# Kernel tuning notes

Measured on AMD Instinct MI355X. Metric: run time of the kernel, lower is better.

## Reference

```python
import jax, jax.numpy as jnp
import numpy as np

WINDOW = 2  # window_size

def _causal_window_conv(x, W, b):
    # x: [B,T,D_in], W: [WINDOW, D_in, D_out], b: [D_out]
    # equivalent to left-padding x by WINDOW-1 zeros and a 'valid' conv
    B, T, _ = x.shape
    xp = jnp.pad(x, ((0, 0), (WINDOW - 1, 0), (0, 0)))  # [B, T+WINDOW-1, D_in]
    out = b
    for k in range(WINDOW):
        out = out + jnp.einsum('btd,de->bte', xp[:, k:k + T], W[k])
    return out  # [B,T,D_out]

def setup_inputs() -> dict:
    key = jax.random.key(0)
    ks = jax.random.split(key, 4)
    B, T, Din, Dout = 8, 4096, 256, 256
    scale = 0.05
    x = jax.random.normal(ks[0], (B, T, Din), dtype=jnp.float32)
    W_z = jax.random.normal(ks[1], (WINDOW, Din, Dout), dtype=jnp.float32) * scale
    W_f = jax.random.normal(ks[2], (WINDOW, Din, Dout), dtype=jnp.float32) * scale
    W_o = jax.random.normal(ks[3], (WINDOW, Din, Dout), dtype=jnp.float32) * scale
    b_z = jnp.zeros((Dout,), dtype=jnp.float32)
    b_f = jnp.zeros((Dout,), dtype=jnp.float32)
    b_o = jnp.zeros((Dout,), dtype=jnp.float32)
    return {"x": x, "W_z": W_z, "W_f": W_f, "W_o": W_o,
            "b_z": b_z, "b_f": b_f, "b_o": b_o}

def reference(x, W_z, W_f, W_o, b_z, b_f, b_o):
    # QRNN with fo-pooling (Bradbury et al. 2016), return_sequences=True
    z = jnp.tanh(_causal_window_conv(x, W_z, b_z))          # [B,T,D]
    f = jax.nn.sigmoid(_causal_window_conv(x, W_f, b_f))    # [B,T,D]
    o = jax.nn.sigmoid(_causal_window_conv(x, W_o, b_o))    # [B,T,D]

    def step(c, zfo):
        z_t, f_t, o_t = zfo
        c = f_t * c + (1.0 - f_t) * z_t   # fo-pooling recurrence
        h = o_t * c
        return c, h

    c0 = jnp.zeros(z.shape[::2], dtype=z.dtype)  # [B,D]
    # time-major for scan
    zfo = (z.transpose(1, 0, 2), f.transpose(1, 0, 2), o.transpose(1, 0, 2))
    _, hs = jax.lax.scan(step, c0, zfo)
    return hs.transpose(1, 0, 2)  # [B,T,D]
```

## Files before the change

kernel.cpp:

```cpp
#include <hip/hip_runtime.h>
#include <hip/hip_bf16.h>
#include <hip/hip_fp16.h>

#define BDIM 8
#define TDIM 4096
#define DDIM 256
#define MDIM (BDIM * TDIM)
#define NCHUNK 256
#define LCHUNK (TDIM / NCHUNK)

typedef _Float16 f16x8 __attribute__((ext_vector_type(8)));
typedef _Float16 f16x4 __attribute__((ext_vector_type(4)));
typedef float f32x4 __attribute__((ext_vector_type(4)));

__device__ __forceinline__ float sigmoid_(float x) {
    return 1.0f / (1.0f + __expf(-x));
}
__device__ __forceinline__ float tanh_(float x) {
    return 2.0f / (1.0f + __expf(-2.0f * x)) - 1.0f;
}

__device__ __forceinline__ f16x8 cvt8(const float4 a, const float4 b) {
    f16x8 r;
    r[0] = (_Float16)a.x; r[1] = (_Float16)a.y;
    r[2] = (_Float16)a.z; r[3] = (_Float16)a.w;
    r[4] = (_Float16)b.x; r[5] = (_Float16)b.y;
    r[6] = (_Float16)b.z; r[7] = (_Float16)b.w;
    return r;
}

__global__ __launch_bounds__(256) void convert_w(
    const float* __restrict__ Wz, const float* __restrict__ Wf,
    const float* __restrict__ Wo, _Float16* __restrict__ Wt) {
    const int idx = blockIdx.x * 256 + threadIdx.x;
    const int n = idx & 255;
    const int kin = (idx >> 8) & 255;
    const int w = (idx >> 16) & 1;
    const int g = idx >> 17;
    const float* W = (g == 0) ? Wz : (g == 1) ? Wf : Wo;
    const float v = W[(size_t)w * 65536 + (size_t)kin * 256 + n];
    Wt[((size_t)g * 256 + n) * 512 + w * 256 + kin] = (_Float16)v;
}

__global__ __launch_bounds__(256) void gates_mfma(
    const float* __restrict__ x, const _Float16* __restrict__ Wt,
    const float* __restrict__ bz, const float* __restrict__ bfv,
    const float* __restrict__ bo,
    _Float16* __restrict__ zbuf, _Float16* __restrict__ fbuf,
    _Float16* __restrict__ obuf) {
    const int gate = blockIdx.z;
    const int m0 = blockIdx.x * 128;
    const int n0 = blockIdx.y * 128;
    const int tid = threadIdx.x;
    const int lane = tid & 63;
    const int wave = tid >> 6;
    const int wr = wave >> 1;
    const int wc = wave & 1;

    __shared__ __align__(16) char smem[40960];

    const int arow = tid >> 1;
    const int ac = (tid & 1) * 16;

    const int b = m0 >> 12;
    const int t0 = m0 & (TDIM - 1);

    const float* xb = x + (size_t)b * TDIM * DDIM;
    const _Float16* pB = Wt + ((size_t)gate * 256 + n0 + arow) * 512 + ac;

    float4 ga0, ga1, ga2, ga3;
    int4 gb0, gb1;

#define LOAD_TILE(k0)                                                        \
    {                                                                        \
        const int half = (k0) >> 8;                                          \
        const int kin = (k0) & 255;                                          \
        const int t = t0 + arow - 1 + half;                                  \
        if (t >= 0) {                                                        \
            const float* src = xb + (size_t)t * DDIM + kin + ac;             \
            ga0 = *(const float4*)(src);                                     \
            ga1 = *(const float4*)(src + 4);                                 \
            ga2 = *(const float4*)(src + 8);                                 \
            ga3 = *(const float4*)(src + 12);                                \
        } else {                                                             \
            ga0 = ga1 = ga2 = ga3 = make_float4(0.f, 0.f, 0.f, 0.f);         \
        }                                                                    \
        gb0 = *(const int4*)(pB + (k0));                                     \
        gb1 = *(const int4*)(pB + (k0) + 8);                                 \
    }

#define STORE_TILE(bufp)                                                     \
    {                                                                        \
        _Float16* Ad = (_Float16*)(bufp);                                    \
        _Float16* Bd = (_Float16*)((char*)(bufp) + 8192);                    \
        *(f16x8*)(Ad + arow * 32 + ac) = cvt8(ga0, ga1);                     \
        *(f16x8*)(Ad + arow * 32 + ac + 8) = cvt8(ga2, ga3);                 \
        *(int4*)(Bd + arow * 32 + ac) = gb0;                                 \
        *(int4*)(Bd + arow * 32 + ac + 8) = gb1;                             \
    }

    f32x4 acc[4][4] = {};
    const int am = lane & 15;
    const int kq = (lane >> 4) * 8;

    LOAD_TILE(0);
    STORE_TILE(smem);

    for (int it = 0; it < 16; ++it) {
        __syncthreads();
        const int cur = it & 1;
        if (it < 15) LOAD_TILE((it + 1) * 32);

        const _Float16* Ab = (const _Float16*)(smem + cur * 16384);
        const _Float16* Bb = (const _Float16*)(smem + cur * 16384 + 8192);

        f16x8 a[4], bb[4];
#pragma unroll
        for (int i = 0; i < 4; ++i)
            a[i] = *(const f16x8*)(Ab + (wr * 64 + i * 16 + am) * 32 + kq);
#pragma unroll
        for (int j = 0; j < 4; ++j)
            bb[j] = *(const f16x8*)(Bb + (wc * 64 + j * 16 + am) * 32 + kq);
#pragma unroll
        for (int i = 0; i < 4; ++i)
#pragma unroll
            for (int j = 0; j < 4; ++j)
                acc[i][j] = __builtin_amdgcn_mfma_f32_16x16x32_f16(
                    a[i], bb[j], acc[i][j], 0, 0, 0);

        if (it < 15) STORE_TILE(smem + (cur ^ 1) * 16384);
    }

    __syncthreads();

    const float* bias = (gate == 0) ? bz : (gate == 1) ? bfv : bo;
    _Float16* outp = (gate == 0) ? zbuf : (gate == 1) ? fbuf : obuf;
    _Float16* eb = (_Float16*)smem + wave * 5120;
    const int rq = (lane >> 4) * 4;
#pragma unroll
    for (int j = 0; j < 4; ++j) {
        const int gc = n0 + wc * 64 + j * 16 + am;
        const float bj = bias[gc];
#pragma unroll
        for (int i = 0; i < 4; ++i) {
            f32x4 v = acc[i][j];
#pragma unroll
            for (int r = 0; r < 4; ++r) {
                const float val = v[r] + bj;
                const float act = (gate == 0) ? tanh_(val) : sigmoid_(val);
                eb[(i * 16 + rq + r) * 80 + j * 16 + am] = (_Float16)act;
            }
        }
    }
    __syncthreads();

    const int rrow = lane >> 3;
    const int rcol = (lane & 7) * 8;
#pragma unroll
    for (int rr = 0; rr < 8; ++rr) {
        const int row = rr * 8 + rrow;
        f16x8 v = *(const f16x8*)(eb + row * 80 + rcol);
        const size_t gm = (size_t)(m0 + wr * 64 + row);
        *(f16x8*)(outp + gm * DDIM + n0 + wc * 64 + rcol) = v;
    }
#undef LOAD_TILE
#undef STORE_TILE
}

__global__ __launch_bounds__(256) void scan_pass1(
    const _Float16* __restrict__ zbuf, const _Float16* __restrict__ fbuf,
    float* __restrict__ aggA, float* __restrict__ aggB) {
    const int idx = blockIdx.x * 256 + threadIdx.x;
    const int d8 = idx & 31;
    const int chunk = (idx >> 5) & (NCHUNK - 1);
    const int b = idx >> 13;

    const size_t row0 = (size_t)b * TDIM + (size_t)chunk * LCHUNK;
    const int4* zp = (const int4*)zbuf + row0 * 32 + d8;
    const int4* fp = (const int4*)fbuf + row0 * 32 + d8;

    float A[8], c[8];
#pragma unroll
    for (int e = 0; e < 8; ++e) { A[e] = 1.0f; c[e] = 0.0f; }

#pragma unroll
    for (int i = 0; i < LCHUNK; ++i) {
        int4 fv = *fp;
        int4 zv = *zp;
        const _Float16* fh = (const _Float16*)&fv;
        const _Float16* zh = (const _Float16*)&zv;
#pragma unroll
        for (int e = 0; e < 8; ++e) {
            const float f = (float)fh[e];
            const float z = (float)zh[e];
            A[e] *= f;
            c[e] = f * c[e] + (1.0f - f) * z;
        }
        fp += 32;
        zp += 32;
    }
    ((float4*)aggA)[(size_t)idx * 2 + 0] = make_float4(A[0], A[1], A[2], A[3]);
    ((float4*)aggA)[(size_t)idx * 2 + 1] = make_float4(A[4], A[5], A[6], A[7]);
    ((float4*)aggB)[(size_t)idx * 2 + 0] = make_float4(c[0], c[1], c[2], c[3]);
    ((float4*)aggB)[(size_t)idx * 2 + 1] = make_float4(c[4], c[5], c[6], c[7]);
}

__global__ __launch_bounds__(256) void carry_scan(
    const float* __restrict__ aggA, const float* __restrict__ aggB,
    float* __restrict__ carry) {
    const int g = blockIdx.x * 256 + threadIdx.x;
    const int d = g & 255;
    const int b = g >> 8;
    const size_t base = (size_t)b * NCHUNK * 256 + d;

    float c = 0.0f;
    for (int ch0 = 0; ch0 < NCHUNK; ch0 += 8) {
        float A[8], Bv[8];
#pragma unroll
        for (int u = 0; u < 8; ++u) {
            const size_t p = base + (size_t)(ch0 + u) * 256;
            A[u] = aggA[p];
            Bv[u] = aggB[p];
        }
#pragma unroll
        for (int u = 0; u < 8; ++u) {
            const size_t p = base + (size_t)(ch0 + u) * 256;
            carry[p] = c;
            c = A[u] * c + Bv[u];
        }
    }
}

__global__ __launch_bounds__(256) void scan_pass2(
    const _Float16* __restrict__ zbuf, const _Float16* __restrict__ fbuf,
    const _Float16* __restrict__ obuf, const float* __restrict__ carry,
    float* __restrict__ out) {
    const int idx = blockIdx.x * 256 + threadIdx.x;
    const int d8 = idx & 31;
    const int chunk = (idx >> 5) & (NCHUNK - 1);
    const int b = idx >> 13;

    float c[8];
    float4 c0 = ((const float4*)carry)[(size_t)idx * 2];
    float4 c1 = ((const float4*)carry)[(size_t)idx * 2 + 1];
    c[0] = c0.x; c[1] = c0.y; c[2] = c0.z; c[3] = c0.w;
    c[4] = c1.x; c[5] = c1.y; c[6] = c1.z; c[7] = c1.w;

    const size_t row0 = (size_t)b * TDIM + (size_t)chunk * LCHUNK;
    const int4* zp = (const int4*)zbuf + row0 * 32 + d8;
    const int4* fp = (const int4*)fbuf + row0 * 32 + d8;
    const int4* op = (const int4*)obuf + row0 * 32 + d8;
    float4* hp = (float4*)out + row0 * 64 + d8 * 2;

#pragma unroll
    for (int i = 0; i < LCHUNK; ++i) {
        int4 fv = *fp;
        int4 zv = *zp;
        int4 ov = *op;
        const _Float16* fh = (const _Float16*)&fv;
        const _Float16* zh = (const _Float16*)&zv;
        const _Float16* oh = (const _Float16*)&ov;
        float h[8];
#pragma unroll
        for (int e = 0; e < 8; ++e) {
            const float f = (float)fh[e];
            const float z = (float)zh[e];
            c[e] = f * c[e] + (1.0f - f) * z;
            h[e] = (float)oh[e] * c[e];
        }
        hp[0] = make_float4(h[0], h[1], h[2], h[3]);
        hp[1] = make_float4(h[4], h[5], h[6], h[7]);
        fp += 32;
        zp += 32;
        op += 32;
        hp += 64;
    }
}

extern "C" void kernel_launch(void* const* d_in, const int* in_sizes, int n_in,
                              void* d_out, int out_size, void* d_ws,
                              size_t ws_size, hipStream_t stream) {
    const float* x = (const float*)d_in[0];
    const float* Wz = (const float*)d_in[1];
    const float* Wf = (const float*)d_in[2];
    const float* Wo = (const float*)d_in[3];
    const float* bz = (const float*)d_in[4];
    const float* bfv = (const float*)d_in[5];
    const float* bo = (const float*)d_in[6];
    float* out = (float*)d_out;

    char* p = (char*)d_ws;
    _Float16* Wt = (_Float16*)p;    p += (size_t)3 * 256 * 512 * 2;
    _Float16* zbuf = (_Float16*)p;  p += (size_t)MDIM * DDIM * 2;
    _Float16* fbuf = (_Float16*)p;  p += (size_t)MDIM * DDIM * 2;
    _Float16* obuf = (_Float16*)p;  p += (size_t)MDIM * DDIM * 2;
    float* aggA = (float*)p;        p += (size_t)BDIM * NCHUNK * DDIM * 4;
    float* aggB = (float*)p;        p += (size_t)BDIM * NCHUNK * DDIM * 4;
    float* carry = (float*)p;

    convert_w<<<(3 * 2 * 256 * 256) / 256, 256, 0, stream>>>(Wz, Wf, Wo, Wt);

    gates_mfma<<<dim3(MDIM / 128, DDIM / 128, 3), 256, 0, stream>>>(
        x, Wt, bz, bfv, bo, zbuf, fbuf, obuf);

    scan_pass1<<<(BDIM * NCHUNK * 32) / 256, 256, 0, stream>>>(zbuf, fbuf,
                                                               aggA, aggB);
    carry_scan<<<(BDIM * DDIM) / 256, 256, 0, stream>>>(aggA, aggB, carry);
    scan_pass2<<<(BDIM * NCHUNK * 32) / 256, 256, 0, stream>>>(zbuf, fbuf,
                                                               obuf, carry, out);
}
```

Measured before the change: 181.3 us.

## Remap gate GEMM blocks for x-tile L2 reuse and shrink LDS footprint

Flattens the 3D grid into a 1D block index, so that the six (gate, n-half) blocks sharing an M tile are scheduled near each other and can reuse the same x rows from L2. Tile loads are reworked so each thread loads 8 contiguous elements from two rows 64 apart, which coalesces better. The epilogue is split into two passes with a smaller padded staging buffer, cutting shared memory from 40KB to 32KB to allow higher occupancy. The cost is an extra barrier pair in the epilogue and more index arithmetic.

New measurement: 186.3 us. 2.7% more time.

```diff
diff --git a/kernel.cpp b/kernel.cpp
--- a/kernel.cpp
+++ b/kernel.cpp
@@ -48,19 +48,23 @@
     const float* __restrict__ bo,
     _Float16* __restrict__ zbuf, _Float16* __restrict__ fbuf,
     _Float16* __restrict__ obuf) {
-    const int gate = blockIdx.z;
-    const int m0 = blockIdx.x * 128;
-    const int n0 = blockIdx.y * 128;
+    const int bid = blockIdx.x;
+    const int mt = (bid & 7) + 8 * (bid / 48);
+    const int g6 = (bid >> 3) % 6;
+    const int gate = g6 >> 1;
+    const int n0 = (g6 & 1) * 128;
+
+    const int m0 = mt * 128;
     const int tid = threadIdx.x;
     const int lane = tid & 63;
     const int wave = tid >> 6;
     const int wr = wave >> 1;
     const int wc = wave & 1;
 
-    __shared__ __align__(16) char smem[40960];
-
-    const int arow = tid >> 1;
-    const int ac = (tid & 1) * 16;
+    __shared__ __align__(16) char smem[32768];
+
+    const int arow = tid >> 2;
+    const int ac = (tid & 3) * 8;
 
     const int b = m0 >> 12;
     const int t0 = m0 & (TDIM - 1);
@@ -74,19 +78,21 @@
 #define LOAD_TILE(k0)                                                        \
     {                                                                        \
         const int half = (k0) >> 8;                                          \
-        const int kin = (k0) & 255;                                          \
-        const int t = t0 + arow - 1 + half;                                  \
-        if (t >= 0) {                                                        \
-            const float* src = xb + (size_t)t * DDIM + kin + ac;             \
-            ga0 = *(const float4*)(src);                                     \
-            ga1 = *(const float4*)(src + 4);                                 \
-            ga2 = *(const float4*)(src + 8);                                 \
-            ga3 = *(const float4*)(src + 12);                                \
+        const int kin = ((k0) & 255) + ac;                                   \
+        const int t1 = t0 + arow - 1 + half;                                 \
+        const int t2 = t1 + 64;                             \
+        if (t1 >= 0) {                                                       \
+            const float* s1 = xb + (size_t)t1 * DDIM + kin;                  \
+            ga0 = *(const float4*)(s1);                                      \
+            ga1 = *(const float4*)(s1 + 4);                                  \
         } else {                                                             \
-            ga0 = ga1 = ga2 = ga3 = make_float4(0.f, 0.f, 0.f, 0.f);         \
+            ga0 = ga1 = make_float4(0.f, 0.f, 0.f, 0.f);                     \
         }                                                                    \
+        const float* s2 = xb + (size_t)t2 * DDIM + kin;                      \
+        ga2 = *(const float4*)(s2);                                          \
+        ga3 = *(const float4*)(s2 + 4);                                      \
         gb0 = *(const int4*)(pB + (k0));                                     \
-        gb1 = *(const int4*)(pB + (k0) + 8);                                 \
+        gb1 = *(const int4*)(pB + (size_t)64 * 512 + (k0));                  \
     }
 
 #define STORE_TILE(bufp)                                                     \
@@ -94,9 +100,9 @@
         _Float16* Ad = (_Float16*)(bufp);                                    \
         _Float16* Bd = (_Float16*)((char*)(bufp) + 8192);                    \
         *(f16x8*)(Ad + arow * 32 + ac) = cvt8(ga0, ga1);                     \
-        *(f16x8*)(Ad + arow * 32 + ac + 8) = cvt8(ga2, ga3);                 \
+        *(f16x8*)(Ad + (arow + 64) * 32 + ac) = cvt8(ga2, ga3);              \
         *(int4*)(Bd + arow * 32 + ac) = gb0;                                 \
-        *(int4*)(Bd + arow * 32 + ac + 8) = gb1;                             \
+        *(int4*)(Bd + (arow + 64) * 32 + ac) = gb1;                          \
     }
 
     f32x4 acc[4][4] = {};
@@ -131,37 +137,40 @@
         if (it < 15) STORE_TILE(smem + (cur ^ 1) * 16384);
     }
 
-    __syncthreads();
-
     const float* bias = (gate == 0) ? bz : (gate == 1) ? bfv : bo;
     _Float16* outp = (gate == 0) ? zbuf : (gate == 1) ? fbuf : obuf;
-    _Float16* eb = (_Float16*)smem + wave * 5120;
+    _Float16* eb = (_Float16*)smem + wave * 2176;
     const int rq = (lane >> 4) * 4;
-#pragma unroll
-    for (int j = 0; j < 4; ++j) {
-        const int gc = n0 + wc * 64 + j * 16 + am;
-        const float bj = bias[gc];
-#pragma unroll
-        for (int i = 0; i < 4; ++i) {
-            f32x4 v = acc[i][j];
-#pragma unroll
-            for (int r = 0; r < 4; ++r) {
-                const float val = v[r] + bj;
-                const float act = (gate == 0) ? tanh_(val) : sigmoid_(val);
-                eb[(i * 16 + rq + r) * 80 + j * 16 + am] = (_Float16)act;
-            }
-        }
-    }
-    __syncthreads();
-
     const int rrow = lane >> 3;
     const int rcol = (lane & 7) * 8;
-#pragma unroll
-    for (int rr = 0; rr < 8; ++rr) {
-        const int row = rr * 8 + rrow;
-        f16x8 v = *(const f16x8*)(eb + row * 80 + rcol);
-        const size_t gm = (size_t)(m0 + wr * 64 + row);
-        *(f16x8*)(outp + gm * DDIM + n0 + wc * 64 + rcol) = v;
+
+#pragma unroll
+    for (int pass = 0; pass < 2; ++pass) {
+        __syncthreads();
+#pragma unroll
+        for (int j = 0; j < 4; ++j) {
+            const int gc = n0 + wc * 64 + j * 16 + am;
+            const float bj = bias[gc];
+#pragma unroll
+            for (int ii = 0; ii < 2; ++ii) {
+                f32x4 v = acc[pass * 2 + ii][j];
+#pragma unroll
+                for (int r = 0; r < 4; ++r) {
+                    const float val = v[r] + bj;
+                    const float act =
+                        (gate == 0) ? tanh_(val) : sigmoid_(val);
+                    eb[(ii * 16 + rq + r) * 68 + j * 16 + am] = (_Float16)act;
+                }
+            }
+        }
+        __syncthreads();
+#pragma unroll
+        for (int rr = 0; rr < 4; ++rr) {
+            const int row = rr * 8 + rrow;
+            f16x8 v = *(const f16x8*)(eb + row * 68 + rcol);
+            const size_t gm = (size_t)(m0 + wr * 64 + pass * 32 + row);
+            *(f16x8*)(outp + gm * DDIM + n0 + wc * 64 + rcol) = v;
+        }
     }
 #undef LOAD_TILE
 #undef STORE_TILE
@@ -300,7 +309,7 @@
 
     convert_w<<<(3 * 2 * 256 * 256) / 256, 256, 0, stream>>>(Wz, Wf, Wo, Wt);
 
-    gates_mfma<<<dim3(MDIM / 128, DDIM / 128, 3), 256, 0, stream>>>(
+    gates_mfma<<<(MDIM / 128) * 2 * 3, 256, 0, stream>>>(
         x, Wt, bz, bfv, bo, zbuf, fbuf, obuf);
 
     scan_pass1<<<(BDIM * NCHUNK * 32) / 256, 256, 0, stream>>>(zbuf, fbuf,
```

## Restructure gate GEMM as persistent kernel with LDS-resident weights and direct-register A loads

Applied to the files above, without the earlier changes.

Replaces the 128x128 double-buffered GEMM tile grid with a 256-block persistent kernel. Each block handles three 256x128 output tiles, stages a 128x256 half-precision weight slab in swizzled LDS per window tap, and streams x directly from global memory into registers for the MFMA A operand. The A loads are software-pipelined across k-steps, and tanh/sigmoid are unified into a single parameterised expression. This removes the A-tile LDS round trip and increases reuse per block. In exchange it uses larger accumulators (occupancy 1), uncoalesced row-strided A loads, and only 256 blocks.

After: 207.1 us. 1.14x slower.

```diff
diff --git a/kernel.cpp b/kernel.cpp
--- a/kernel.cpp
+++ b/kernel.cpp
@@ -10,14 +10,10 @@
 #define LCHUNK (TDIM / NCHUNK)
 
 typedef _Float16 f16x8 __attribute__((ext_vector_type(8)));
-typedef _Float16 f16x4 __attribute__((ext_vector_type(4)));
 typedef float f32x4 __attribute__((ext_vector_type(4)));
 
 __device__ __forceinline__ float sigmoid_(float x) {
     return 1.0f / (1.0f + __expf(-x));
-}
-__device__ __forceinline__ float tanh_(float x) {
-    return 2.0f / (1.0f + __expf(-2.0f * x)) - 1.0f;
 }
 
 __device__ __forceinline__ f16x8 cvt8(const float4 a, const float4 b) {
@@ -42,129 +38,155 @@
     Wt[((size_t)g * 256 + n) * 512 + w * 256 + kin] = (_Float16)v;
 }
 
-__global__ __launch_bounds__(256) void gates_mfma(
+__global__ __launch_bounds__(256, 1) void gates_mfma(
     const float* __restrict__ x, const _Float16* __restrict__ Wt,
     const float* __restrict__ bz, const float* __restrict__ bfv,
     const float* __restrict__ bo,
     _Float16* __restrict__ zbuf, _Float16* __restrict__ fbuf,
     _Float16* __restrict__ obuf) {
-    const int gate = blockIdx.z;
-    const int m0 = blockIdx.x * 128;
-    const int n0 = blockIdx.y * 128;
     const int tid = threadIdx.x;
     const int lane = tid & 63;
     const int wave = tid >> 6;
-    const int wr = wave >> 1;
-    const int wc = wave & 1;
-
-    __shared__ __align__(16) char smem[40960];
-
-    const int arow = tid >> 1;
-    const int ac = (tid & 1) * 16;
-
-    const int b = m0 >> 12;
-    const int t0 = m0 & (TDIM - 1);
-
-    const float* xb = x + (size_t)b * TDIM * DDIM;
-    const _Float16* pB = Wt + ((size_t)gate * 256 + n0 + arow) * 512 + ac;
-
-    float4 ga0, ga1, ga2, ga3;
-    int4 gb0, gb1;
-
-#define LOAD_TILE(k0)                                                        \
+
+    __shared__ __align__(16) char smem[65536];
+    _Float16* Bs = (_Float16*)smem;
+
+    const int am = lane & 15;
+    const int lq = lane >> 4;
+    const int kq = lq * 8;
+    const int amx = am & 7;
+
+    const int scol = tid & 127;
+    const int sck = (tid >> 7) * 16;
+
+    for (int jr = 0; jr < 3; ++jr) {
+        const int j = blockIdx.x + jr * 256;
+        const int gate = j >> 8;
+        const int n0 = ((j >> 7) & 1) * 128;
+        const int m0 = (j & 127) * 256;
+        const int b = m0 >> 12;
+        const int t0 = m0 & (TDIM - 1);
+        const float* xb = x + (size_t)b * TDIM * DDIM;
+
+        f32x4 acc[4][8] = {};
+
+        const int twave = t0 + wave * 64;
+        const bool edge = (t0 == 0) && (wave == 0);
+
+        for (int pass = 0; pass < 2; ++pass) {
+            __syncthreads();
+            {
+                const _Float16* src =
+                    Wt + ((size_t)gate * 256 + n0 + scol) * 512 + pass * 256 +
+                    sck * 8;
+                int4 r[16];
+#pragma unroll
+                for (int i = 0; i < 16; ++i) r[i] = ((const int4*)src)[i];
+                _Float16* dstc = Bs + scol * 256;
+#pragma unroll
+                for (int i = 0; i < 16; ++i)
+                    *(int4*)(dstc + (((sck + i) ^ (scol & 7)) << 3)) = r[i];
+            }
+            __syncthreads();
+
+            const float* arow[4];
+#pragma unroll
+            for (int rf = 0; rf < 4; ++rf)
+                arow[rf] = xb +
+                           ((long)(twave + rf * 16 + am) - 1 + pass) * DDIM +
+                           kq;
+            const bool ep = edge && (pass == 0);
+
+            float4 A0[4][2], A1[4][2];
+
+#define LOADA(dst, ks8)                                                      \
     {                                                                        \
-        const int half = (k0) >> 8;                                          \
-        const int kin = (k0) & 255;                                          \
-        const int t = t0 + arow - 1 + half;                                  \
-        if (t >= 0) {                                                        \
-            const float* src = xb + (size_t)t * DDIM + kin + ac;             \
-            ga0 = *(const float4*)(src);                                     \
-            ga1 = *(const float4*)(src + 4);                                 \
-            ga2 = *(const float4*)(src + 8);                                 \
-            ga3 = *(const float4*)(src + 12);                                \
-        } else {                                                             \
-            ga0 = ga1 = ga2 = ga3 = make_float4(0.f, 0.f, 0.f, 0.f);         \
+        const int kb = (ks8)*32;                                             \
+        _Pragma("unroll") for (int rf = 0; rf < 4; ++rf) {                   \
+            dst[rf][0] = *(const float4*)(arow[rf] + kb);                    \
+            dst[rf][1] = *(const float4*)(arow[rf] + kb + 4);                 \
         }                                                                    \
-        gb0 = *(const int4*)(pB + (k0));                                     \
-        gb1 = *(const int4*)(pB + (k0) + 8);                                 \
-    }
-
-#define STORE_TILE(bufp)                                                     \
+    }
+#define LOADA_EDGE(dst, ks8)                                                 \
     {                                                                        \
-        _Float16* Ad = (_Float16*)(bufp);                                    \
-        _Float16* Bd = (_Float16*)((char*)(bufp) + 8192);                    \
-        *(f16x8*)(Ad + arow * 32 + ac) = cvt8(ga0, ga1);                     \
-        *(f16x8*)(Ad + arow * 32 + ac + 8) = cvt8(ga2, ga3);                 \
-        *(int4*)(Bd + arow * 32 + ac) = gb0;                                 \
-        *(int4*)(Bd + arow * 32 + ac + 8) = gb1;                             \
-    }
-
-    f32x4 acc[4][4] = {};
-    const int am = lane & 15;
-    const int kq = (lane >> 4) * 8;
-
-    LOAD_TILE(0);
-    STORE_TILE(smem);
-
-    for (int it = 0; it < 16; ++it) {
+        const int kb = (ks8)*32;                                             \
+        _Pragma("unroll") for (int rf = 0; rf < 4; ++rf) {                   \
+            if (rf == 0 && am == 0) {                                        \
+                dst[rf][0] = make_float4(0.f, 0.f, 0.f, 0.f);                \
+                dst[rf][1] = make_float4(0.f, 0.f, 0.f, 0.f);                \
+            } else {                                                         \
+                dst[rf][0] = *(const float4*)(arow[rf] + kb);                \
+                dst[rf][1] = *(const float4*)(arow[rf] + kb + 4);             \
+            }                                                                \
+        }                                                                    \
+    }
+#define DOMFMA(Abuf, ks8)                                                    \
+    {                                                                        \
+        f16x8 bb[8];                                                         \
+        _Pragma("unroll") for (int cf = 0; cf < 8; ++cf) {                   \
+            const int col = cf * 16 + am;                                    \
+            const int ch = ((ks8)*4 + lq) ^ amx;                             \
+            bb[cf] = *(const f16x8*)(Bs + col * 256 + ch * 8);               \
+        }                                                                    \
+        f16x8 aa[4];                                                         \
+        _Pragma("unroll") for (int rf = 0; rf < 4; ++rf) aa[rf] =            \
+            cvt8(Abuf[rf][0], Abuf[rf][1]);                                  \
+        _Pragma("unroll") for (int rf = 0; rf < 4; ++rf)                     \
+            _Pragma("unroll") for (int cf = 0; cf < 8; ++cf) acc[rf][cf] =   \
+                __builtin_amdgcn_mfma_f32_16x16x32_f16(aa[rf], bb[cf],       \
+                                                       acc[rf][cf], 0, 0, 0);\
+    }
+
+            if (ep) { LOADA_EDGE(A0, 0) } else { LOADA(A0, 0) }
+            for (int ks8 = 0; ks8 < 8; ks8 += 2) {
+                if (ep) { LOADA_EDGE(A1, ks8 + 1) } else { LOADA(A1, ks8 + 1) }
+                DOMFMA(A0, ks8)
+                if (ks8 + 2 < 8) {
+                    if (ep) { LOADA_EDGE(A0, ks8 + 2) } else { LOADA(A0, ks8 + 2) }
+                }
+                DOMFMA(A1, ks8 + 1)
+            }
+#undef LOADA
+#undef LOADA_EDGE
+#undef DOMFMA
+        }
+
         __syncthreads();
-        const int cur = it & 1;
-        if (it < 15) LOAD_TILE((it + 1) * 32);
-
-        const _Float16* Ab = (const _Float16*)(smem + cur * 16384);
-        const _Float16* Bb = (const _Float16*)(smem + cur * 16384 + 8192);
-
-        f16x8 a[4], bb[4];
-#pragma unroll
-        for (int i = 0; i < 4; ++i)
-            a[i] = *(const f16x8*)(Ab + (wr * 64 + i * 16 + am) * 32 + kq);
-#pragma unroll
-        for (int j = 0; j < 4; ++j)
-            bb[j] = *(const f16x8*)(Bb + (wc * 64 + j * 16 + am) * 32 + kq);
-#pragma unroll
-        for (int i = 0; i < 4; ++i)
-#pragma unroll
-            for (int j = 0; j < 4; ++j)
-                acc[i][j] = __builtin_amdgcn_mfma_f32_16x16x32_f16(
-                    a[i], bb[j], acc[i][j], 0, 0, 0);
-
-        if (it < 15) STORE_TILE(smem + (cur ^ 1) * 16384);
-    }
-
-    __syncthreads();
-
-    const float* bias = (gate == 0) ? bz : (gate == 1) ? bfv : bo;
-    _Float16* outp = (gate == 0) ? zbuf : (gate == 1) ? fbuf : obuf;
-    _Float16* eb = (_Float16*)smem + wave * 5120;
-    const int rq = (lane >> 4) * 4;
-#pragma unroll
-    for (int j = 0; j < 4; ++j) {
-        const int gc = n0 + wc * 64 + j * 16 + am;
-        const float bj = bias[gc];
-#pragma unroll
-        for (int i = 0; i < 4; ++i) {
-            f32x4 v = acc[i][j];
-#pragma unroll
-            for (int r = 0; r < 4; ++r) {
-                const float val = v[r] + bj;
-                const float act = (gate == 0) ? tanh_(val) : sigmoid_(val);
-                eb[(i * 16 + rq + r) * 80 + j * 16 + am] = (_Float16)act;
+        const float* bias = (gate == 0) ? bz : (gate == 1) ? bfv : bo;
+        _Float16* outp = (gate == 0) ? zbuf : (gate == 1) ? fbuf : obuf;
+        const float amul = (gate == 0) ? 2.f : 1.f;
+        const float smul = (gate == 0) ? -2.f : -1.f;
+        const float asub = (gate == 0) ? 1.f : 0.f;
+
+        _Float16* eb = (_Float16*)smem + wave * 8192;
+        float bj[8];
+#pragma unroll
+        for (int cf = 0; cf < 8; ++cf) bj[cf] = bias[n0 + cf * 16 + am];
+        const int rq = lq * 4;
+#pragma unroll
+        for (int rf = 0; rf < 4; ++rf)
+#pragma unroll
+            for (int cf = 0; cf < 8; ++cf) {
+                f32x4 v = acc[rf][cf];
+#pragma unroll
+                for (int r = 0; r < 4; ++r) {
+                    const float val = v[r] + bj[cf];
+                    const float act =
+                        amul / (1.f + __expf(smul * val)) - asub;
+                    eb[(rf * 16 + rq + r) * 128 + cf * 16 + am] =
+                        (_Float16)act;
+                }
             }
-        }
-    }
-    __syncthreads();
-
-    const int rrow = lane >> 3;
-    const int rcol = (lane & 7) * 8;
-#pragma unroll
-    for (int rr = 0; rr < 8; ++rr) {
-        const int row = rr * 8 + rrow;
-        f16x8 v = *(const f16x8*)(eb + row * 80 + rcol);
-        const size_t gm = (size_t)(m0 + wr * 64 + row);
-        *(f16x8*)(outp + gm * DDIM + n0 + wc * 64 + rcol) = v;
-    }
-#undef LOAD_TILE
-#undef STORE_TILE
+#pragma unroll
+        for (int i = 0; i < 16; ++i) {
+            const int flat = i * 64 + lane;
+            const int row = flat >> 4;
+            const int ch = flat & 15;
+            f16x8 v = *(const f16x8*)(eb + row * 128 + ch * 8);
+            *(f16x8*)(outp + (size_t)(m0 + wave * 64 + row) * DDIM + n0 +
+                      ch * 8) = v;
+        }
+    }
 }
 
 __global__ __launch_bounds__(256) void scan_pass1(
@@ -300,8 +322,7 @@
 
     convert_w<<<(3 * 2 * 256 * 256) / 256, 256, 0, stream>>>(Wz, Wf, Wo, Wt);
 
-    gates_mfma<<<dim3(MDIM / 128, DDIM / 128, 3), 256, 0, stream>>>(
-        x, Wt, bz, bfv, bo, zbuf, fbuf, obuf);
+    gates_mfma<<<256, 256, 0, stream>>>(x, Wt, bz, bfv, bo, zbuf, fbuf, obuf);
 
     scan_pass1<<<(BDIM * NCHUNK * 32) / 256, 256, 0, stream>>>(zbuf, fbuf,
                                                                aggA, aggB);
```

## Fuse three-pass chunked scan into single decoupled-lookback scan kernel

Applied to the files above, without the earlier changes.

Replaces the three scan kernels (chunk aggregate, serial carry scan, and apply) with one kernel. Each block handles 128 timesteps of one batch across all 256 features, publishes its aggregate and an inclusive prefix through flags, and looks back over earlier chunks to get its entering state. This removes two kernel launches and the aggA/carry round trips, but adds a hipMemsetAsync for the flags. It relies on forward-progress ordering of blocks (only 256 blocks) and drops parallelism from 2048 to 256 blocks with scalar fp16 loads, which may lower bandwidth use.

Result: slower. 401.0 us (+121.2%).

```diff
diff --git a/kernel.cpp b/kernel.cpp
--- a/kernel.cpp
+++ b/kernel.cpp
@@ -6,11 +6,10 @@
 #define TDIM 4096
 #define DDIM 256
 #define MDIM (BDIM * TDIM)
-#define NCHUNK 256
-#define LCHUNK (TDIM / NCHUNK)
+#define SCHUNK 128
+#define NCH (TDIM / SCHUNK)
 
 typedef _Float16 f16x8 __attribute__((ext_vector_type(8)));
-typedef _Float16 f16x4 __attribute__((ext_vector_type(4)));
 typedef float f32x4 __attribute__((ext_vector_type(4)));
 
 __device__ __forceinline__ float sigmoid_(float x) {
@@ -167,113 +166,100 @@
 #undef STORE_TILE
 }
 
-__global__ __launch_bounds__(256) void scan_pass1(
+__global__ __launch_bounds__(256) void scan_fused(
     const _Float16* __restrict__ zbuf, const _Float16* __restrict__ fbuf,
-    float* __restrict__ aggA, float* __restrict__ aggB) {
-    const int idx = blockIdx.x * 256 + threadIdx.x;
-    const int d8 = idx & 31;
-    const int chunk = (idx >> 5) & (NCHUNK - 1);
-    const int b = idx >> 13;
-
-    const size_t row0 = (size_t)b * TDIM + (size_t)chunk * LCHUNK;
-    const int4* zp = (const int4*)zbuf + row0 * 32 + d8;
-    const int4* fp = (const int4*)fbuf + row0 * 32 + d8;
-
-    float A[8], c[8];
-#pragma unroll
-    for (int e = 0; e < 8; ++e) { A[e] = 1.0f; c[e] = 0.0f; }
-
-#pragma unroll
-    for (int i = 0; i < LCHUNK; ++i) {
-        int4 fv = *fp;
-        int4 zv = *zp;
-        const _Float16* fh = (const _Float16*)&fv;
-        const _Float16* zh = (const _Float16*)&zv;
-#pragma unroll
-        for (int e = 0; e < 8; ++e) {
-            const float f = (float)fh[e];
-            const float z = (float)zh[e];
-            A[e] *= f;
-            c[e] = f * c[e] + (1.0f - f) * z;
-        }
-        fp += 32;
-        zp += 32;
-    }
-    ((float4*)aggA)[(size_t)idx * 2 + 0] = make_float4(A[0], A[1], A[2], A[3]);
-    ((float4*)aggA)[(size_t)idx * 2 + 1] = make_float4(A[4], A[5], A[6], A[7]);
-    ((float4*)aggB)[(size_t)idx * 2 + 0] = make_float4(c[0], c[1], c[2], c[3]);
-    ((float4*)aggB)[(size_t)idx * 2 + 1] = make_float4(c[4], c[5], c[6], c[7]);
-}
-
-__global__ __launch_bounds__(256) void carry_scan(
-    const float* __restrict__ aggA, const float* __restrict__ aggB,
-    float* __restrict__ carry) {
-    const int g = blockIdx.x * 256 + threadIdx.x;
-    const int d = g & 255;
-    const int b = g >> 8;
-    const size_t base = (size_t)b * NCHUNK * 256 + d;
-
-    float c = 0.0f;
-    for (int ch0 = 0; ch0 < NCHUNK; ch0 += 8) {
-        float A[8], Bv[8];
-#pragma unroll
-        for (int u = 0; u < 8; ++u) {
-            const size_t p = base + (size_t)(ch0 + u) * 256;
-            A[u] = aggA[p];
-            Bv[u] = aggB[p];
-        }
-#pragma unroll
-        for (int u = 0; u < 8; ++u) {
-            const size_t p = base + (size_t)(ch0 + u) * 256;
-            carry[p] = c;
-            c = A[u] * c + Bv[u];
-        }
-    }
-}
-
-__global__ __launch_bounds__(256) void scan_pass2(
-    const _Float16* __restrict__ zbuf, const _Float16* __restrict__ fbuf,
-    const _Float16* __restrict__ obuf, const float* __restrict__ carry,
-    float* __restrict__ out) {
-    const int idx = blockIdx.x * 256 + threadIdx.x;
-    const int d8 = idx & 31;
-    const int chunk = (idx >> 5) & (NCHUNK - 1);
-    const int b = idx >> 13;
-
-    float c[8];
-    float4 c0 = ((const float4*)carry)[(size_t)idx * 2];
-    float4 c1 = ((const float4*)carry)[(size_t)idx * 2 + 1];
-    c[0] = c0.x; c[1] = c0.y; c[2] = c0.z; c[3] = c0.w;
-    c[4] = c1.x; c[5] = c1.y; c[6] = c1.z; c[7] = c1.w;
-
-    const size_t row0 = (size_t)b * TDIM + (size_t)chunk * LCHUNK;
-    const int4* zp = (const int4*)zbuf + row0 * 32 + d8;
-    const int4* fp = (const int4*)fbuf + row0 * 32 + d8;
-    const int4* op = (const int4*)obuf + row0 * 32 + d8;
-    float4* hp = (float4*)out + row0 * 64 + d8 * 2;
-
-#pragma unroll
-    for (int i = 0; i < LCHUNK; ++i) {
-        int4 fv = *fp;
-        int4 zv = *zp;
-        int4 ov = *op;
-        const _Float16* fh = (const _Float16*)&fv;
-        const _Float16* zh = (const _Float16*)&zv;
-        const _Float16* oh = (const _Float16*)&ov;
-        float h[8];
-#pragma unroll
-        for (int e = 0; e < 8; ++e) {
-            const float f = (float)fh[e];
-            const float z = (float)zh[e];
-            c[e] = f * c[e] + (1.0f - f) * z;
-            h[e] = (float)oh[e] * c[e];
-        }
-        hp[0] = make_float4(h[0], h[1], h[2], h[3]);
-        hp[1] = make_float4(h[4], h[5], h[6], h[7]);
-        fp += 32;
-        zp += 32;
-        op += 32;
-        hp += 64;
+    const _Float16* __restrict__ obuf, float* __restrict__ aggA,
+    float* __restrict__ aggB, float* __restrict__ aggI,
+    int* __restrict__ flags, float* __restrict__ out) {
+    const int bid = blockIdx.x;
+    const int b = bid >> 5;
+    const int chunk = bid & (NCH - 1);
+    const int d = threadIdx.x;
+    const size_t base = ((size_t)b * TDIM + (size_t)chunk * SCHUNK) * DDIM + d;
+
+    float A = 1.0f, c = 0.0f;
+    for (int i = 0; i < SCHUNK; i += 4) {
+        float ff[4], zz[4];
+#pragma unroll
+        for (int u = 0; u < 4; ++u) {
+            ff[u] = (float)fbuf[base + (size_t)(i + u) * DDIM];
+            zz[u] = (float)zbuf[base + (size_t)(i + u) * DDIM];
+        }
+#pragma unroll
+        for (int u = 0; u < 4; ++u) {
+            A *= ff[u];
+            c = ff[u] * c + (1.0f - ff[u]) * zz[u];
+        }
+    }
+
+    __shared__ int st_sh;
+    float c_enter = 0.0f;
+
+    if (chunk == 0) {
+        aggI[bid * 256 + d] = c;
+        __threadfence();
+        __syncthreads();
+        if (d == 0)
+            __hip_atomic_store(&flags[bid], 2, __ATOMIC_RELEASE,
+                               __HIP_MEMORY_SCOPE_AGENT);
+    } else {
+        aggA[bid * 256 + d] = A;
+        aggB[bid * 256 + d] = c;
+        __threadfence();
+        __syncthreads();
+        if (d == 0)
+            __hip_atomic_store(&flags[bid], 1, __ATOMIC_RELEASE,
+                               __HIP_MEMORY_SCOPE_AGENT);
+
+        float accA = 1.0f, accB = 0.0f;
+        for (int j = chunk - 1; j >= 0; --j) {
+            if (d == 0) {
+                int s;
+                do {
+                    s = __hip_atomic_load(&flags[(b << 5) + j],
+                                          __ATOMIC_ACQUIRE,
+                                          __HIP_MEMORY_SCOPE_AGENT);
+                    if (s == 0) __builtin_amdgcn_s_sleep(1);
+                } while (s == 0);
+                st_sh = s;
+            }
+            __syncthreads();
+            const int s = st_sh;
+            __threadfence();
+            if (s == 2) {
+                const float v = aggI[((b << 5) + j) * 256 + d];
+                c_enter = accA * v + accB;
+                break;
+            }
+            const float Aj = aggA[((b << 5) + j) * 256 + d];
+            const float Bj = aggB[((b << 5) + j) * 256 + d];
+            accB = accB + accA * Bj;
+            accA = accA * Aj;
+            __syncthreads();
+        }
+
+        aggI[bid * 256 + d] = A * c_enter + c;
+        __threadfence();
+        __syncthreads();
+        if (d == 0)
+            __hip_atomic_store(&flags[bid], 2, __ATOMIC_RELEASE,
+                               __HIP_MEMORY_SCOPE_AGENT);
+    }
+
+    float c2 = c_enter;
+    for (int i = 0; i < SCHUNK; i += 4) {
+        float ff[4], zz[4], oo[4];
+#pragma unroll
+        for (int u = 0; u < 4; ++u) {
+            ff[u] = (float)fbuf[base + (size_t)(i + u) * DDIM];
+            zz[u] = (float)zbuf[base + (size_t)(i + u) * DDIM];
+            oo[u] = (float)obuf[base + (size_t)(i + u) * DDIM];
+        }
+#pragma unroll
+        for (int u = 0; u < 4; ++u) {
+            c2 = ff[u] * c2 + (1.0f - ff[u]) * zz[u];
+            out[base + (size_t)(i + u) * DDIM] = oo[u] * c2;
+        }
     }
 }
 
@@ -294,18 +280,18 @@
     _Float16* zbuf = (_Float16*)p;  p += (size_t)MDIM * DDIM * 2;
     _Float16* fbuf = (_Float16*)p;  p += (size_t)MDIM * DDIM * 2;
     _Float16* obuf = (_Float16*)p;  p += (size_t)MDIM * DDIM * 2;
-    float* aggA = (float*)p;        p += (size_t)BDIM * NCHUNK * DDIM * 4;
-    float* aggB = (float*)p;        p += (size_t)BDIM * NCHUNK * DDIM * 4;
-    float* carry = (float*)p;
+    float* aggA = (float*)p;        p += (size_t)BDIM * NCH * 256 * 4;
+    float* aggB = (float*)p;        p += (size_t)BDIM * NCH * 256 * 4;
+    float* aggI = (float*)p;        p += (size_t)BDIM * NCH * 256 * 4;
+    int* flags = (int*)p;
 
     convert_w<<<(3 * 2 * 256 * 256) / 256, 256, 0, stream>>>(Wz, Wf, Wo, Wt);
 
     gates_mfma<<<dim3(MDIM / 128, DDIM / 128, 3), 256, 0, stream>>>(
         x, Wt, bz, bfv, bo, zbuf, fbuf, obuf);
 
-    scan_pass1<<<(BDIM * NCHUNK * 32) / 256, 256, 0, stream>>>(zbuf, fbuf,
-                                                               aggA, aggB);
-    carry_scan<<<(BDIM * DDIM) / 256, 256, 0, stream>>>(aggA, aggB, carry);
-    scan_pass2<<<(BDIM * NCHUNK * 32) / 256, 256, 0, stream>>>(zbuf, fbuf,
-                                                               obuf, carry, out);
-}
+    hipMemsetAsync(flags, 0, BDIM * NCH * sizeof(int), stream);
+
+    scan_fused<<<BDIM * NCH, 256, 0, stream>>>(zbuf, fbuf, obuf, aggA, aggB,
+                                               aggI, flags, out);
+}
```
